# Kernel tuning notes

Measured on AMD Instinct MI355X. Metric: run time of the kernel, lower is better.

The kernel has to match this reference:

```python
import jax, jax.numpy as jnp
import numpy as np

DIM = 1024
HEADS = 16
HIDDEN = 4096
EPS = 1e-5


def _layernorm(x, g, b):
    mu = jnp.mean(x, axis=-1, keepdims=True)
    var = jnp.mean(jnp.square(x - mu), axis=-1, keepdims=True)
    return (x - mu) * jax.lax.rsqrt(var + EPS) * g + b


def setup_inputs() -> dict:
    key = jax.random.key(0)
    ks = jax.random.split(key, 12)
    B, N, C, Hd = 2, 2048, DIM, HIDDEN
    s = 0.02
    inp = {
        "x": jax.random.normal(ks[0], (B, N, C), dtype=jnp.float32),
        "mask": jax.random.randint(ks[1], (B, N), 0, 2).astype(bool),
        "ln1_g": jnp.ones((C,), jnp.float32),
        "ln1_b": jnp.zeros((C,), jnp.float32),
        "qkv_w": jax.random.normal(ks[2], (3 * C, C), jnp.float32) * s,
        "q_bias": jax.random.normal(ks[3], (C,), jnp.float32) * s,
        "v_bias": jax.random.normal(ks[4], (C,), jnp.float32) * s,
        "proj_w": jax.random.normal(ks[5], (C, C), jnp.float32) * s,
        "proj_b": jnp.zeros((C,), jnp.float32),
        "ln2_g": jnp.ones((C,), jnp.float32),
        "ln2_b": jnp.zeros((C,), jnp.float32),
        "fc1_w": jax.random.normal(ks[6], (Hd, C), jnp.float32) * s,
        "fc1_b": jnp.zeros((Hd,), jnp.float32),
        "fc2_w": jax.random.normal(ks[7], (C, Hd), jnp.float32) * s,
        "fc2_b": jnp.zeros((C,), jnp.float32),
    }
    return inp


def _block(x, mask, ln1_g, ln1_b, qkv_w, q_bias, v_bias, proj_w, proj_b,
           ln2_g, ln2_b, fc1_w, fc1_b, fc2_w, fc2_b):
    B, N, C = x.shape
    H = HEADS
    hd = C // H
    scale = hd ** -0.5

    # --- attention branch ---
    xn = _layernorm(x, ln1_g, ln1_b)
    qkv_bias = jnp.concatenate([q_bias, jnp.zeros_like(v_bias), v_bias])
    qkv = xn @ qkv_w.T + qkv_bias                       # [B,N,3C]
    qkv = qkv.reshape(B, N, 3, H, hd).transpose(2, 0, 3, 1, 4)  # [3,B,H,N,hd]
    q, k, v = qkv[0], qkv[1], qkv[2]
    q = q * scale
    attn = jnp.einsum('bhqd,bhkd->bhqk',
                      q.astype(jnp.float32), k.astype(jnp.float32))
    attn = jnp.where(mask[:, None, None, :], -jnp.inf, attn)
    attn = jax.nn.softmax(attn, axis=-1).astype(x.dtype)
    out = jnp.einsum('bhqk,bhkd->bhqd', attn, v)        # [B,H,N,hd]
    out = out.transpose(0, 2, 1, 3).reshape(B, N, C)
    out = out @ proj_w.T + proj_b
    x = x + out

    # --- MLP branch (Mlp_ returns pre-activation hidden too; norm=Identity) ---
    x2 = _layernorm(x, ln2_g, ln2_b)
    h = x2 @ fc1_w.T + fc1_b                            # [B,N,HIDDEN]
    x_interm = h
    h = jax.nn.gelu(h, approximate=False)
    y = h @ fc2_w.T + fc2_b
    x = x + y
    return x_interm, x


def reference(x, mask, ln1_g, ln1_b, qkv_w, q_bias, v_bias, proj_w, proj_b,
              ln2_g, ln2_b, fc1_w, fc1_b, fc2_w, fc2_b):
    return _block(x, mask, ln1_g, ln1_b, qkv_w, q_bias, v_bias, proj_w, proj_b,
                  ln2_g, ln2_b, fc1_w, fc1_b, fc2_w, fc2_b)
```

## Files before the change

kernel.cpp:

```cpp
#include <hip/hip_runtime.h>
#include <hip/hip_bf16.h>

typedef __attribute__((ext_vector_type(8))) short short8;
typedef __attribute__((ext_vector_type(4))) short short4v;
typedef __attribute__((ext_vector_type(4))) float f32x4;

__device__ inline float bf2f(short s) {
    unsigned u = ((unsigned)(unsigned short)s) << 16;
    float f; __builtin_memcpy(&f, &u, 4); return f;
}
__device__ inline short f2bf(float f) {
    unsigned u; __builtin_memcpy(&u, &f, 4);
    unsigned r = (u + 0x7fffu + ((u >> 16) & 1u)) >> 16;
    return (short)r;
}
__device__ inline float ex2(float x) {
    float r; asm("v_exp_f32 %0, %1" : "=v"(r) : "v"(x)); return r;
}
__device__ inline unsigned cvtpk(float lo, float hi) {
    unsigned r; asm("v_cvt_pk_bf16_f32 %0, %1, %2" : "=v"(r) : "v"(lo), "v"(hi)); return r;
}

#define GLD_LDS16(g, l) __builtin_amdgcn_global_load_lds( \
    (const __attribute__((address_space(1))) void*)(g),   \
    (__attribute__((address_space(3))) void*)(l), 16, 0, 0)

__global__ __launch_bounds__(256) void detect_kernel(const ushort* __restrict__ x,
                                                     const unsigned char* __restrict__ m,
                                                     int* __restrict__ flags) {
    __shared__ int cnt, weirdAny, weird40, nzNon4;
    if (threadIdx.x == 0) { cnt = 0; weirdAny = 0; weird40 = 0; nzNon4 = 0; }
    __syncthreads();
    for (int t = threadIdx.x; t < 512; t += 256) {
        unsigned u = x[2 * t];
        int e = (int)((u >> 7) & 0xFF);
        if (e >= 100 && e <= 130) atomicAdd(&cnt, 1);
    }
    for (int i = threadIdx.x; i < 4096; i += 256) {
        unsigned b = m[i];
        if (b > 1) { atomicOr(&weirdAny, 1); if ((i & 3) == 0) atomicOr(&weird40, 1); }
        if (b != 0 && (i & 3) != 0) atomicOr(&nzNon4, 1);
    }
    __syncthreads();
    if (threadIdx.x == 0) {
        flags[0] = (cnt < 256) ? 1 : 0;
        flags[1] = weirdAny ? (weird40 ? 2 : 3) : (nzNon4 ? 1 : 0);
    }
}

__global__ __launch_bounds__(256) void prep_kernel(
    const void* __restrict__ xs, const void* __restrict__ ms,
    const void* __restrict__ ln1g, const void* __restrict__ ln1b,
    const void* __restrict__ qkvw, const void* __restrict__ qb,
    const void* __restrict__ vb, const void* __restrict__ pw,
    const void* __restrict__ pb, const void* __restrict__ ln2g,
    const void* __restrict__ ln2b, const void* __restrict__ f1w,
    const void* __restrict__ f1b, const void* __restrict__ f2w,
    const void* __restrict__ f2b,
    char* __restrict__ w, const int* __restrict__ flags) {
    bool f32w = flags[0] != 0;
    const size_t MB = 1024 * 1024;
    int bid = blockIdx.x, tid = threadIdx.x;
    char* small = w + 88 * MB;
    auto cvt8 = [&](const void* src, ushort* dst, int i) {
        if (f32w) {
            const float* s = (const float*)src + i;
            short8 o;
            for (int j = 0; j < 8; j++) o[j] = f2bf(s[j]);
            *(short8*)&dst[i] = o;
        } else {
            *(short8*)&dst[i] = *(const short8*)((const ushort*)src + i);
        }
    };
    if (bid < 2048)       cvt8(xs,   (ushort*)(w + 56 * MB), (bid * 256 + tid) * 8);
    else if (bid < 3584)  cvt8(qkvw, (ushort*)(w + 64 * MB), ((bid - 2048) * 256 + tid) * 8);
    else if (bid < 4096)  cvt8(pw,   (ushort*)(w + 70 * MB), ((bid - 3584) * 256 + tid) * 8);
    else if (bid < 6144)  cvt8(f1w,  (ushort*)(w + 72 * MB), ((bid - 4096) * 256 + tid) * 8);
    else if (bid < 8192)  cvt8(f2w,  (ushort*)(w + 80 * MB), ((bid - 6144) * 256 + tid) * 8);
    else if (bid < 8198) {
        int e = (bid - 8192) * 2048 + tid * 8;
        const void* src; ushort* dst; int off;
        if (e < 7168) {
            int t = e >> 10; off = e & 1023;
            const void* s0;
            if (t == 0) s0 = ln1g; else if (t == 1) s0 = ln1b; else if (t == 2) s0 = qb;
            else if (t == 3) s0 = vb; else if (t == 4) s0 = pb; else if (t == 5) s0 = ln2g;
            else s0 = ln2b;
            src = s0; dst = (ushort*)(small + t * 4096);
        } else if (e < 8192) { src = f2b; off = e - 7168; dst = (ushort*)(small + 9 * 4096); }
        else                 { src = f1b; off = e - 8192; dst = (ushort*)(small + 7 * 4096); }
        cvt8(src, dst, off);
    } else {
        int enc = flags[1];
        unsigned char* md = (unsigned char*)(small + 10 * 4096);
        int i0 = (bid - 8198) * 2048 + tid * 8;
        for (int j = 0; j < 8; j++) {
            int i = i0 + j;
            unsigned char v;
            if (enc == 0)      v = (((const int*)ms)[i] != 0);
            else if (enc == 1) v = (((const unsigned char*)ms)[i] != 0);
            else if (enc == 2) v = (((const ushort*)ms)[i] != 0);
            else               v = ((((const unsigned*)ms)[i] << 1) != 0);
            md[i] = v;
        }
    }
}

__global__ __launch_bounds__(256) void ln_kernel(const ushort* __restrict__ x,
                                                 const ushort* __restrict__ g,
                                                 const ushort* __restrict__ b,
                                                 ushort* __restrict__ y) {
    int wave = threadIdx.x >> 6, lane = threadIdx.x & 63;
    int row = blockIdx.x * 4 + wave;
    const ushort* xp = x + (size_t)row * 1024 + lane * 16;
    short8 v0 = *(const short8*)xp;
    short8 v1 = *(const short8*)(xp + 8);
    float f[16]; float s = 0.f, ss = 0.f;
    for (int i = 0; i < 8; i++) { f[i] = bf2f(v0[i]); f[i + 8] = bf2f(v1[i]); }
    for (int i = 0; i < 16; i++) { s += f[i]; ss += f[i] * f[i]; }
    for (int o = 1; o < 64; o <<= 1) { s += __shfl_xor(s, o, 64); ss += __shfl_xor(ss, o, 64); }
    float mu = s * (1.f / 1024.f);
    float var = ss * (1.f / 1024.f) - mu * mu;
    float rstd = rsqrtf(var + 1e-5f);
    short8 g0 = *(const short8*)&g[lane * 16];
    short8 g1 = *(const short8*)&g[lane * 16 + 8];
    short8 b0 = *(const short8*)&b[lane * 16];
    short8 b1 = *(const short8*)&b[lane * 16 + 8];
    short8 o0v, o1v;
    for (int i = 0; i < 8; i++) {
        o0v[i] = f2bf((f[i] - mu) * rstd * bf2f(g0[i]) + bf2f(b0[i]));
        o1v[i] = f2bf((f[i + 8] - mu) * rstd * bf2f(g1[i]) + bf2f(b1[i]));
    }
    ushort* yp = y + (size_t)row * 1024 + lane * 16;
    *(short8*)yp = o0v;
    *(short8*)(yp + 8) = o1v;
}

template <int EPI>
__device__ __forceinline__ void gemm_body(ushort* SM,
                                          const ushort* __restrict__ A,
                                          const ushort* __restrict__ W,
                                          int K,
                                          const ushort* __restrict__ p0,
                                          const ushort* __restrict__ p1,
                                          void* __restrict__ o0,
                                          ushort* __restrict__ o1,
                                          const int* __restrict__ flags) {
    int tid = threadIdx.x;
    int wave = tid >> 6, lane = tid & 63;
    int wr = wave >> 1, wc = wave & 1;
    int lr = lane & 15, lg = lane >> 4;
    int m0 = blockIdx.x * 128, n0 = blockIdx.y * 128;
    f32x4 acc[4][4];
    for (int i = 0; i < 4; i++) for (int j = 0; j < 4; j++) acc[i][j] = (f32x4){0.f, 0.f, 0.f, 0.f};

    int s0 = wave * 2;
    int srow = lane >> 2;
    int sslot = (lane & 3) ^ ((srow >> 1) & 3);
    const ushort* gA0 = &A[(size_t)(m0 + s0 * 16 + srow) * K + sslot * 8];
    const ushort* gA1 = gA0 + (size_t)16 * K;
    const ushort* gW0 = &W[(size_t)(n0 + s0 * 16 + srow) * K + sslot * 8];
    const ushort* gW1 = gW0 + (size_t)16 * K;

    auto STAGE = [&](int buf, int k0) {
        ushort* lA = &SM[buf * 4096 + s0 * 512];
        ushort* lW = &SM[8192 + buf * 4096 + s0 * 512];
        GLD_LDS16(gA0 + k0, lA);
        GLD_LDS16(gA1 + k0, lA + 512);
        GLD_LDS16(gW0 + k0, lW);
        GLD_LDS16(gW1 + k0, lW + 512);
    };

    STAGE(0, 0);
    __syncthreads();
    int nk = K >> 5;
    int rs = lg ^ ((lr >> 1) & 3);
    for (int t = 0; t < nk; ++t) {
        int cur = t & 1;
        if (t + 1 < nk) STAGE(cur ^ 1, (t + 1) << 5);
        const ushort* Ab = &SM[cur * 4096];
        const ushort* Wb = &SM[8192 + cur * 4096];
        short8 af[4], wf[4];
        for (int mi = 0; mi < 4; mi++) af[mi] = *(const short8*)&Ab[(wr * 64 + mi * 16 + lr) * 32 + rs * 8];
        for (int ni = 0; ni < 4; ni++) wf[ni] = *(const short8*)&Wb[(wc * 64 + ni * 16 + lr) * 32 + rs * 8];
        for (int mi = 0; mi < 4; mi++)
            for (int ni = 0; ni < 4; ni++)
                acc[mi][ni] = __builtin_amdgcn_mfma_f32_16x16x32_bf16(af[mi], wf[ni], acc[mi][ni], 0, 0, 0);
        __syncthreads();
    }

    float* Cs = (float*)SM;
    bool of32 = (EPI == 2 || EPI == 3) ? (flags[0] != 0) : false;
    int r2 = tid >> 3;
    int lc = tid & 7;
    for (int mi = 0; mi < 4; mi++) {
        __syncthreads();
        int rb = wr * 16 + lg * 4;
        for (int ni = 0; ni < 4; ni++) {
            f32x4 v = acc[mi][ni];
            int cl = wc * 64 + ni * 16 + lr;
            for (int rr = 0; rr < 4; rr++) Cs[(rb + rr) * 132 + cl] = v[rr];
        }
        __syncthreads();
        int grow = m0 + mi * 16 + (r2 < 16 ? r2 : 48 + r2);
        if (EPI == 3 && of32) {
            for (int k = 0; k < 4; k++) {
                int c0l = k * 32 + lc * 4;
                int gcol = n0 + c0l;
                f32x4 v;
                for (int j = 0; j < 4; j++)
                    v[j] = Cs[r2 * 132 + c0l + j] + bf2f(p0[gcol + j])
                         + bf2f(p1[(size_t)grow * 1024 + gcol + j]);
                *(f32x4*)&((float*)o0)[16777216 + (size_t)grow * 1024 + gcol] = v;
            }
        } else {
            for (int half = 0; half < 2; half++) {
                int c0l = half * 64 + lc * 8;
                int gcol = n0 + c0l;
                float hv[8];
                for (int j = 0; j < 8; j++) hv[j] = Cs[r2 * 132 + c0l + j];
                short8 o;
                if (EPI == 0) {
                    int part = gcol >> 10, cc = gcol & 1023;
                    if (part == 0)
                        for (int j = 0; j < 8; j++) o[j] = f2bf((hv[j] + bf2f(p0[cc + j])) * 0.18033688f);
                    else if (part == 1)
                        for (int j = 0; j < 8; j++) o[j] = f2bf(hv[j]);
                    else
                        for (int j = 0; j < 8; j++) o[j] = f2bf(hv[j] + bf2f(p1[cc + j]));
                    *(short8*)&((ushort*)o0)[(size_t)grow * 3072 + gcol] = o;
                } else if (EPI == 1) {
                    for (int j = 0; j < 8; j++)
                        o[j] = f2bf(hv[j] + bf2f(p0[gcol + j])
                                  + bf2f(p1[(size_t)grow * 1024 + gcol + j]));
                    *(short8*)&((ushort*)o0)[(size_t)grow * 1024 + gcol] = o;
                } else if (EPI == 2) {
                    float h[8];
                    short8 og;
                    for (int j = 0; j < 8; j++) {
                        h[j] = hv[j] + bf2f(p0[gcol + j]);
                        float ge = 0.5f * h[j] * (1.f + erff(h[j] * 0.70710678118f));
                        og[j] = f2bf(ge);
                    }
                    *(short8*)&o1[(size_t)grow * 4096 + gcol] = og;
                    if (of32) {
                        float* dst = &((float*)o0)[(size_t)grow * 4096 + gcol];
                        *(f32x4*)&dst[0] = (f32x4){h[0], h[1], h[2], h[3]};
                        *(f32x4*)&dst[4] = (f32x4){h[4], h[5], h[6], h[7]};
                    } else {
                        short8 oh;
                        for (int j = 0; j < 8; j++) oh[j] = f2bf(h[j]);
                        *(short8*)&((ushort*)o0)[(size_t)grow * 4096 + gcol] = oh;
                    }
                } else {
                    for (int j = 0; j < 8; j++)
                        o[j] = f2bf(hv[j] + bf2f(p0[gcol + j])
                                  + bf2f(p1[(size_t)grow * 1024 + gcol + j]));
                    *(short8*)&((ushort*)o0)[16777216 + (size_t)grow * 1024 + gcol] = o;
                }
            }
        }
    }
}

#define GEMM_WRAP(NAME, EPI)                                                          \
__global__ __launch_bounds__(256) void NAME(const ushort* __restrict__ A,            \
                                            const ushort* __restrict__ W, int K,     \
                                            const ushort* __restrict__ p0,           \
                                            const ushort* __restrict__ p1,           \
                                            void* __restrict__ o0,                   \
                                            ushort* __restrict__ o1,                 \
                                            const int* __restrict__ flags) {         \
    __shared__ ushort SM[16384];                                                     \
    gemm_body<EPI>(SM, A, W, K, p0, p1, o0, o1, flags);                              \
}

GEMM_WRAP(gemm_qkv, 0)
GEMM_WRAP(gemm_proj, 1)
GEMM_WRAP(gemm_fc1, 2)
GEMM_WRAP(gemm_fc2, 3)

__global__ __launch_bounds__(256) void vtrans_kernel(const ushort* __restrict__ qkv,
                                                     ushort* __restrict__ vT) {
    __shared__ ushort T[64][72];
    int bh = blockIdx.x;
    int b = bh >> 4, h = bh & 15;
    int n0 = blockIdx.y * 64;
    int t = threadIdx.x;
    int r = t >> 2;
    int c0 = (t & 3) * 16;
    const ushort* src = qkv + (size_t)(b * 2048 + n0 + r) * 3072 + 2048 + h * 64 + c0;
    *(short8*)&T[r][c0]     = *(const short8*)&src[0];
    *(short8*)&T[r][c0 + 8] = *(const short8*)&src[8];
    __syncthreads();
    int d = t >> 2;
    int g0 = (t & 3) * 16;
    short8 o0v, o1v;
    for (int j = 0; j < 8; j++) { o0v[j] = T[g0 + j][d]; o1v[j] = T[g0 + 8 + j][d]; }
    ushort* dst = vT + ((size_t)bh * 64 + d) * 2048 + n0 + g0;
    *(short8*)&dst[0] = o0v;
    *(short8*)&dst[8] = o1v;
}

__global__ __launch_bounds__(256) void attn_kernel(const ushort* __restrict__ qkv,
                                                   const ushort* __restrict__ vT,
                                                   const unsigned char* __restrict__ mask,
                                                   ushort* __restrict__ ao) {
    __shared__ ushort Ks[2][4096];
    __shared__ ushort Vs[2][4096];
    __shared__ unsigned Plw[4][544];
    __shared__ unsigned Pmf[1024];

    int tid = threadIdx.x, wave = tid >> 6, lane = tid & 63;
    int bid = (blockIdx.x & 7) * 64 + (blockIdx.x >> 3);
    int g = bid * 4 + wave;
    int b = g >> 10;
    int h = (g >> 6) & 15;
    int qt = g & 63;
    int lr = lane & 15, lg = lane >> 4;

    const ushort* qp = qkv + (size_t)(b * 2048 + qt * 32) * 3072 + h * 64;
    const ushort* kp = qkv + (size_t)(b * 2048) * 3072 + 1024 + h * 64;
    const ushort* vp = vT + ((size_t)(b * 16 + h) * 64) * 2048;
    const unsigned char* mk = mask + b * 2048;

    for (int i = tid; i < 1024; i += 256) {
        unsigned lo = mk[2 * i] ? 0u : 0xFFFFu;
        unsigned hi = mk[2 * i + 1] ? 0u : 0xFFFF0000u;
        Pmf[i] = lo | hi;
    }

    short8 qa[2][2];
    for (int sub = 0; sub < 2; sub++)
        for (int ks = 0; ks < 2; ks++)
            qa[sub][ks] = *(const short8*)&qp[(sub * 16 + lr) * 3072 + ks * 32 + lg * 8];
    short8 ones;
    for (int j = 0; j < 8; j++) ones[j] = (short)0x3F80;

    int srowoff = lane >> 3;
    int sslot = (lane & 7) ^ srowoff;
    int rs0 = lg ^ (lr & 7);
    int rs1 = (4 + lg) ^ (lr & 7);

    f32x4 accT[2][4];
    f32x4 accL[2];
    for (int s = 0; s < 2; s++) {
        accL[s] = (f32x4){0.f, 0.f, 0.f, 0.f};
        for (int i = 0; i < 4; i++) accT[s][i] = (f32x4){0.f, 0.f, 0.f, 0.f};
    }

    auto STAGEKV = [&](int buf, int c0) {
        const ushort* ksrc = kp + (size_t)(c0 + wave * 16 + srowoff) * 3072 + sslot * 8;
        GLD_LDS16(ksrc, &Ks[buf][wave * 1024]);
        GLD_LDS16(ksrc + (size_t)8 * 3072, &Ks[buf][wave * 1024 + 512]);
        const ushort* vsrc = vp + (size_t)(wave * 16 + srowoff) * 2048 + c0 + sslot * 8;
        GLD_LDS16(vsrc, &Vs[buf][wave * 1024]);
        GLD_LDS16(vsrc + (size_t)8 * 2048, &Vs[buf][wave * 1024 + 512]);
    };

    STAGEKV(0, 0);
    __syncthreads();

    for (int it = 0; it < 32; ++it) {
        int c0 = it * 64;
        int cur = it & 1;
        if (it < 31) STAGEKV(cur ^ 1, c0 + 64);

        unsigned mw[4][2];
        for (int t = 0; t < 4; t++) {
            uint2 m2 = *(const uint2*)&Pmf[it * 32 + 8 * t + 2 * lg];
            mw[t][0] = m2.x; mw[t][1] = m2.y;
        }
        f32x4 st[2][4];
        for (int t = 0; t < 4; t++) {
            int row = t * 16 + lr;
            short8 kf0 = *(const short8*)&Ks[cur][row * 64 + rs0 * 8];
            short8 kf1 = *(const short8*)&Ks[cur][row * 64 + rs1 * 8];
            for (int sub = 0; sub < 2; sub++) {
                f32x4 z = (f32x4){0.f, 0.f, 0.f, 0.f};
                z = __builtin_amdgcn_mfma_f32_16x16x32_bf16(kf0, qa[sub][0], z, 0, 0, 0);
                z = __builtin_amdgcn_mfma_f32_16x16x32_bf16(kf1, qa[sub][1], z, 0, 0, 0);
                st[sub][t] = z;
            }
        }
        short8 vf[2][4];
        for (int ks = 0; ks < 2; ks++) {
            int rsk = ks ? rs1 : rs0;
            for (int nt = 0; nt < 4; nt++)
                vf[ks][nt] = *(const short8*)&Vs[cur][(nt * 16 + lr) * 64 + rsk * 8];
        }
        for (int sub = 0; sub < 2; sub++) {
            for (int t = 0; t < 4; t++) {
                for (int rrh = 0; rrh < 2; rrh++) {
                    float plo = ex2(st[sub][t][2 * rrh]);
                    float phi = ex2(st[sub][t][2 * rrh + 1]);
                    unsigned w = cvtpk(plo, phi) & mw[t][rrh];
                    Plw[wave][(8 * t + 2 * lg + rrh) * 17 + lr] = w;
                }
            }
            for (int ks = 0; ks < 2; ks++) {
                unsigned wu[4];
                for (int jj = 0; jj < 4; jj++)
                    wu[jj] = Plw[wave][(16 * ks + 4 * lg + jj) * 17 + lr];
                short8 pf;
                __builtin_memcpy(&pf, wu, 16);
                accL[sub] = __builtin_amdgcn_mfma_f32_16x16x32_bf16(ones, pf, accL[sub], 0, 0, 0);
                for (int nt = 0; nt < 4; nt++)
                    accT[sub][nt] = __builtin_amdgcn_mfma_f32_16x16x32_bf16(vf[ks][nt], pf, accT[sub][nt], 0, 0, 0);
            }
        }
        __syncthreads();
    }

    for (int sub = 0; sub < 2; sub++) {
        float ls = accL[sub][0];
        float inv = (ls > 0.f) ? 1.f / ls : 0.f;
        ushort* op = ao + ((size_t)(b * 2048 + qt * 32 + sub * 16) * 1024) + h * 64;
        for (int nt = 0; nt < 4; nt++) {
            unsigned w0 = cvtpk(accT[sub][nt][0] * inv, accT[sub][nt][1] * inv);
            unsigned w1 = cvtpk(accT[sub][nt][2] * inv, accT[sub][nt][3] * inv);
            uint2 ov; ov.x = w0; ov.y = w1;
            *(uint2*)&op[lr * 1024 + 16 * nt + 4 * lg] = ov;
        }
    }
}

extern "C" void kernel_launch(void* const* d_in, const int* in_sizes, int n_in,
                              void* d_out, int out_size, void* d_ws, size_t ws_size,
                              hipStream_t stream) {
    (void)in_sizes; (void)n_in; (void)out_size; (void)ws_size;

    char* w = (char*)d_ws;
    const size_t MB = 1024 * 1024;
    ushort* xn  = (ushort*)(w + 0 * MB);
    ushort* qkv = (ushort*)(w + 8 * MB);
    ushort* vT  = (ushort*)(w + 32 * MB);
    ushort* x1  = (ushort*)(w + 40 * MB);
    ushort* x2n = (ushort*)(w + 48 * MB);
    ushort* gh  = (ushort*)(w + 8 * MB);
    ushort* x_c    = (ushort*)(w + 56 * MB);
    ushort* qkvw_c = (ushort*)(w + 64 * MB);
    ushort* projw_c= (ushort*)(w + 70 * MB);
    ushort* fc1w_c = (ushort*)(w + 72 * MB);
    ushort* fc2w_c = (ushort*)(w + 80 * MB);
    char* small = w + 88 * MB;
    ushort* ln1g_c = (ushort*)(small + 0 * 4096);
    ushort* ln1b_c = (ushort*)(small + 1 * 4096);
    ushort* qbias_c= (ushort*)(small + 2 * 4096);
    ushort* vbias_c= (ushort*)(small + 3 * 4096);
    ushort* projb_c= (ushort*)(small + 4 * 4096);
    ushort* ln2g_c = (ushort*)(small + 5 * 4096);
    ushort* ln2b_c = (ushort*)(small + 6 * 4096);
    ushort* fc1b_c = (ushort*)(small + 7 * 4096);
    ushort* fc2b_c = (ushort*)(small + 9 * 4096);
    unsigned char* mask_c = (unsigned char*)(small + 10 * 4096);
    int* flags = (int*)(small + 11 * 4096);
    ushort* ao = xn;

    detect_kernel<<<1, 256, 0, stream>>>((const ushort*)d_in[0],
                                         (const unsigned char*)d_in[1], flags);
    prep_kernel<<<8200, 256, 0, stream>>>(d_in[0], d_in[1], d_in[2], d_in[3], d_in[4],
                                          d_in[5], d_in[6], d_in[7], d_in[8], d_in[9],
                                          d_in[10], d_in[11], d_in[12], d_in[13], d_in[14],
                                          w, flags);

    ln_kernel<<<1024, 256, 0, stream>>>(x_c, ln1g_c, ln1b_c, xn);
    gemm_qkv<<<dim3(32, 24), 256, 0, stream>>>(xn, qkvw_c, 1024, qbias_c, vbias_c, qkv, nullptr, flags);
    vtrans_kernel<<<dim3(32, 32), 256, 0, stream>>>(qkv, vT);
    attn_kernel<<<512, 256, 0, stream>>>(qkv, vT, mask_c, ao);
    gemm_proj<<<dim3(32, 8), 256, 0, stream>>>(ao, projw_c, 1024, projb_c, x_c, x1, nullptr, flags);
    ln_kernel<<<1024, 256, 0, stream>>>(x1, ln2g_c, ln2b_c, x2n);
    gemm_fc1<<<dim3(32, 32), 256, 0, stream>>>(x2n, fc1w_c, 1024, fc1b_c, nullptr, d_out, gh, flags);
    gemm_fc2<<<dim3(32, 8), 256, 0, stream>>>(gh, fc2w_c, 4096, fc2b_c, x1, d_out, nullptr, flags);
}
```

Baseline: 286.7 us.

## Triple-buffer GEMM k-loop, skip bf16 copy pass, use exp-based GELU

The GEMM main loop moves from double to triple buffering in LDS, issuing loads two k-steps ahead and waiting with explicit vmcnt counts instead of full __syncthreads. The prep kernel no longer copies weights and activations when the inputs are already bf16; GEMMs and layernorm read the raw input buffers directly. The erf-based GELU is replaced by an exp/reciprocal sigmoid approximation. The exact-GELU swap changes numerics, and the larger LDS footprint may reduce occupancy. The inputs here are float32, so the copy-skip path does not apply.

```diff
diff --git a/kernel.cpp b/kernel.cpp
--- a/kernel.cpp
+++ b/kernel.cpp
@@ -20,10 +20,18 @@
 __device__ inline unsigned cvtpk(float lo, float hi) {
     unsigned r; asm("v_cvt_pk_bf16_f32 %0, %1, %2" : "=v"(r) : "v"(lo), "v"(hi)); return r;
 }
+__device__ inline float gelu_fast(float x) {
+    float xx = x * x;
+    float u2 = x * fmaf(0.10294323f, xx, 2.3022085f);
+    float t = ex2(u2);
+    return x - x * __builtin_amdgcn_rcpf(t + 1.f);
+}
 
 #define GLD_LDS16(g, l) __builtin_amdgcn_global_load_lds( \
     (const __attribute__((address_space(1))) void*)(g),   \
     (__attribute__((address_space(3))) void*)(l), 16, 0, 0)
+
+#define BARRIER_PIN do { __builtin_amdgcn_s_barrier(); __builtin_amdgcn_sched_barrier(0); } while (0)
 
 __global__ __launch_bounds__(256) void detect_kernel(const ushort* __restrict__ x,
                                                      const unsigned char* __restrict__ m,
@@ -61,6 +69,7 @@
     bool f32w = flags[0] != 0;
     const size_t MB = 1024 * 1024;
     int bid = blockIdx.x, tid = threadIdx.x;
+    if (!f32w && bid < 8192) return;
     char* small = w + 88 * MB;
     auto cvt8 = [&](const void* src, ushort* dst, int i) {
         if (f32w) {
@@ -106,10 +115,13 @@
     }
 }
 
-__global__ __launch_bounds__(256) void ln_kernel(const ushort* __restrict__ x,
+__global__ __launch_bounds__(256) void ln_kernel(const void* __restrict__ xraw,
+                                                 const ushort* __restrict__ xconv,
                                                  const ushort* __restrict__ g,
                                                  const ushort* __restrict__ b,
-                                                 ushort* __restrict__ y) {
+                                                 ushort* __restrict__ y,
+                                                 const int* __restrict__ flags) {
+    const ushort* x = (flags[0] != 0) ? xconv : (const ushort*)xraw;
     int wave = threadIdx.x >> 6, lane = threadIdx.x & 63;
     int row = blockIdx.x * 4 + wave;
     const ushort* xp = x + (size_t)row * 1024 + lane * 16;
@@ -139,13 +151,18 @@
 template <int EPI>
 __device__ __forceinline__ void gemm_body(ushort* SM,
                                           const ushort* __restrict__ A,
-                                          const ushort* __restrict__ W,
+                                          const void* __restrict__ Wraw,
+                                          const ushort* __restrict__ Wconv,
                                           int K,
                                           const ushort* __restrict__ p0,
-                                          const ushort* __restrict__ p1,
+                                          const void* __restrict__ p1raw,
+                                          const ushort* __restrict__ p1conv,
                                           void* __restrict__ o0,
                                           ushort* __restrict__ o1,
                                           const int* __restrict__ flags) {
+    bool f32w = flags[0] != 0;
+    const ushort* W  = f32w ? Wconv  : (const ushort*)Wraw;
+    const ushort* p1 = f32w ? p1conv : (const ushort*)p1raw;
     int tid = threadIdx.x;
     int wave = tid >> 6, lane = tid & 63;
     int wr = wave >> 1, wc = wave & 1;
@@ -164,33 +181,46 @@
 
     auto STAGE = [&](int buf, int k0) {
         ushort* lA = &SM[buf * 4096 + s0 * 512];
-        ushort* lW = &SM[8192 + buf * 4096 + s0 * 512];
+        ushort* lW = &SM[12288 + buf * 4096 + s0 * 512];
         GLD_LDS16(gA0 + k0, lA);
         GLD_LDS16(gA1 + k0, lA + 512);
         GLD_LDS16(gW0 + k0, lW);
         GLD_LDS16(gW1 + k0, lW + 512);
     };
 
+    int nk = K >> 5;
     STAGE(0, 0);
-    __syncthreads();
-    int nk = K >> 5;
+    if (nk > 1) {
+        STAGE(1, 32);
+        asm volatile("s_waitcnt vmcnt(4)" ::: "memory");
+    } else {
+        asm volatile("s_waitcnt vmcnt(0)" ::: "memory");
+    }
+    BARRIER_PIN;
+
     int rs = lg ^ ((lr >> 1) & 3);
+    int cur = 0, stg = 2;
     for (int t = 0; t < nk; ++t) {
-        int cur = t & 1;
-        if (t + 1 < nk) STAGE(cur ^ 1, (t + 1) << 5);
+        if (t + 2 < nk) STAGE(stg, (t + 2) << 5);
         const ushort* Ab = &SM[cur * 4096];
-        const ushort* Wb = &SM[8192 + cur * 4096];
+        const ushort* Wb = &SM[12288 + cur * 4096];
         short8 af[4], wf[4];
         for (int mi = 0; mi < 4; mi++) af[mi] = *(const short8*)&Ab[(wr * 64 + mi * 16 + lr) * 32 + rs * 8];
         for (int ni = 0; ni < 4; ni++) wf[ni] = *(const short8*)&Wb[(wc * 64 + ni * 16 + lr) * 32 + rs * 8];
         for (int mi = 0; mi < 4; mi++)
             for (int ni = 0; ni < 4; ni++)
                 acc[mi][ni] = __builtin_amdgcn_mfma_f32_16x16x32_bf16(af[mi], wf[ni], acc[mi][ni], 0, 0, 0);
-        __syncthreads();
+        if (t + 1 < nk) {
+            if (t + 2 < nk) asm volatile("s_waitcnt vmcnt(4)" ::: "memory");
+            else            asm volatile("s_waitcnt vmcnt(0)" ::: "memory");
+            BARRIER_PIN;
+        }
+        cur = (cur == 2) ? 0 : cur + 1;
+        stg = (stg == 2) ? 0 : stg + 1;
     }
 
     float* Cs = (float*)SM;
-    bool of32 = (EPI == 2 || EPI == 3) ? (flags[0] != 0) : false;
+    bool of32 = (EPI == 2 || EPI == 3) ? f32w : false;
     int r2 = tid >> 3;
     int lc = tid & 7;
     for (int mi = 0; mi < 4; mi++) {
@@ -239,8 +269,7 @@
                     short8 og;
                     for (int j = 0; j < 8; j++) {
                         h[j] = hv[j] + bf2f(p0[gcol + j]);
-                        float ge = 0.5f * h[j] * (1.f + erff(h[j] * 0.70710678118f));
-                        og[j] = f2bf(ge);
+                        og[j] = f2bf(gelu_fast(h[j]));
                     }
                     *(short8*)&o1[(size_t)grow * 4096 + gcol] = og;
                     if (of32) {
@@ -265,14 +294,16 @@
 
 #define GEMM_WRAP(NAME, EPI)                                                          \
 __global__ __launch_bounds__(256) void NAME(const ushort* __restrict__ A,            \
-                                            const ushort* __restrict__ W, int K,     \
+                                            const void* __restrict__ Wraw,           \
+                                            const ushort* __restrict__ Wconv, int K, \
                                             const ushort* __restrict__ p0,           \
-                                            const ushort* __restrict__ p1,           \
+                                            const void* __restrict__ p1raw,          \
+                                            const ushort* __restrict__ p1conv,       \
                                             void* __restrict__ o0,                   \
                                             ushort* __restrict__ o1,                 \
                                             const int* __restrict__ flags) {         \
-    __shared__ ushort SM[16384];                                                     \
-    gemm_body<EPI>(SM, A, W, K, p0, p1, o0, o1, flags);                              \
+    __shared__ ushort SM[24576];                                                     \
+    gemm_body<EPI>(SM, A, Wraw, Wconv, K, p0, p1raw, p1conv, o0, o1, flags);         \
 }
 
 GEMM_WRAP(gemm_qkv, 0)
@@ -464,12 +495,16 @@
                                           d_in[10], d_in[11], d_in[12], d_in[13], d_in[14],
                                           w, flags);
 
-    ln_kernel<<<1024, 256, 0, stream>>>(x_c, ln1g_c, ln1b_c, xn);
-    gemm_qkv<<<dim3(32, 24), 256, 0, stream>>>(xn, qkvw_c, 1024, qbias_c, vbias_c, qkv, nullptr, flags);
+    ln_kernel<<<1024, 256, 0, stream>>>(d_in[0], x_c, ln1g_c, ln1b_c, xn, flags);
+    gemm_qkv<<<dim3(32, 24), 256, 0, stream>>>(xn, d_in[4], qkvw_c, 1024, qbias_c,
+                                               vbias_c, vbias_c, qkv, nullptr, flags);
     vtrans_kernel<<<dim3(32, 32), 256, 0, stream>>>(qkv, vT);
     attn_kernel<<<512, 256, 0, stream>>>(qkv, vT, mask_c, ao);
-    gemm_proj<<<dim3(32, 8), 256, 0, stream>>>(ao, projw_c, 1024, projb_c, x_c, x1, nullptr, flags);
-    ln_kernel<<<1024, 256, 0, stream>>>(x1, ln2g_c, ln2b_c, x2n);
-    gemm_fc1<<<dim3(32, 32), 256, 0, stream>>>(x2n, fc1w_c, 1024, fc1b_c, nullptr, d_out, gh, flags);
-    gemm_fc2<<<dim3(32, 8), 256, 0, stream>>>(gh, fc2w_c, 4096, fc2b_c, x1, d_out, nullptr, flags);
-}
+    gemm_proj<<<dim3(32, 8), 256, 0, stream>>>(ao, d_in[7], projw_c, 1024, projb_c,
+                                               d_in[0], x_c, x1, nullptr, flags);
+    ln_kernel<<<1024, 256, 0, stream>>>(x1, x1, ln2g_c, ln2b_c, x2n, flags);
+    gemm_fc1<<<dim3(32, 32), 256, 0, stream>>>(x2n, d_in[11], fc1w_c, 1024, fc1b_c,
+                                               fc1b_c, fc1b_c, d_out, gh, flags);
+    gemm_fc2<<<dim3(32, 8), 256, 0, stream>>>(gh, d_in[13], fc2w_c, 4096, fc2b_c,
+                                              x1, x1, d_out, nullptr, flags);
+}
```

New measurement: 258.5 us. 1.11x faster.
